# Kernel optimization log

Hardware: AMD Instinct MI355X
Metric: run time of the kernel (lower is better)

The kernel has to match this reference:

```python
import jax, jax.numpy as jnp
import numpy as np

B, N, D, H = 2, 2048, 1024, 16
HD = D // H

def setup_inputs() -> dict:
    key = jax.random.key(0)
    ks = jax.random.split(key, 8)
    s = lambda fan_in: 1.0 / np.sqrt(fan_in)
    return {
        "x": jax.random.normal(ks[0], (B, N, D), jnp.float32),
        "coverage": jax.random.uniform(ks[1], (B, N, 1), jnp.float32),
        "w_qkv": jax.random.normal(ks[2], (D, 3 * D), jnp.float32) * s(D),
        "w_out": jax.random.normal(ks[3], (D, D), jnp.float32) * s(D),
        "b_out": jnp.zeros((D,), jnp.float32),
        "w_ce1": jax.random.normal(ks[4], (1, D // 4), jnp.float32),
        "b_ce1": jnp.zeros((D // 4,), jnp.float32),
        "w_ce2": jax.random.normal(ks[5], (D // 4, H), jnp.float32) * s(D // 4),
        "b_ce2": jnp.zeros((H,), jnp.float32),
        "w_fg1": jax.random.normal(ks[6], (D, D // 4), jnp.float32) * s(D),
        "b_fg1": jnp.zeros((D // 4,), jnp.float32),
        "w_fg2": jax.random.normal(ks[7], (D // 4, 1), jnp.float32) * s(D // 4),
        "b_fg2": jnp.zeros((1,), jnp.float32),
    }

def reference(x, coverage, w_qkv, w_out, b_out, w_ce1, b_ce1, w_ce2, b_ce2,
              w_fg1, b_fg1, w_fg2, b_fg2):
    b, n, d = x.shape
    h = w_ce2.shape[1]
    hd = d // h
    scale = hd ** -0.5
    qkv = x @ w_qkv  # (B,N,3D)
    q, k, v = jnp.split(qkv, 3, axis=-1)
    q = q.reshape(b, n, h, hd).transpose(0, 2, 1, 3)  # (B,H,N,hd)
    k = k.reshape(b, n, h, hd).transpose(0, 2, 1, 3)
    v = v.reshape(b, n, h, hd).transpose(0, 2, 1, 3)
    attn = jnp.einsum("bhnd,bhmd->bhnm", q, k) * scale  # (B,H,N,N)
    # coverage bias: MLP(1 -> D/4 -> H), broadcast over query dim
    cov = jax.nn.silu(coverage @ w_ce1 + b_ce1) @ w_ce2 + b_ce2  # (B,N,H)
    cov_bias = cov.transpose(0, 2, 1)[:, :, None, :]  # (B,H,1,N)
    # fusion gate on mean-pooled features
    x_pooled = x.mean(axis=1)  # (B,D)
    g = jax.nn.sigmoid(jax.nn.silu(x_pooled @ w_fg1 + b_fg1) @ w_fg2 + b_fg2)  # (B,1)
    g = g[:, :, None, None]  # (B,1,1,1)
    # g*(attn+bias) + (1-g)*attn == attn + g*bias (exact same math)
    attn = attn + g * cov_bias
    attn = jax.nn.softmax(attn, axis=-1)
    out = jnp.einsum("bhnm,bhmd->bhnd", attn, v)  # (B,H,N,hd)
    out = out.transpose(0, 2, 1, 3).reshape(b, n, d)
    return out @ w_out + b_out
```

## Files before the change

### kernel.cpp

```cpp
#include <hip/hip_runtime.h>
#include <math.h>

typedef __bf16 bf16_t;
typedef __bf16 bf16x8 __attribute__((ext_vector_type(8)));
typedef __bf16 bf16x4 __attribute__((ext_vector_type(4)));
typedef float f32x4 __attribute__((ext_vector_type(4)));

#define MFMA16(a, b, c) __builtin_amdgcn_mfma_f32_16x16x32_bf16((a), (b), (c), 0, 0, 0)

constexpr int Bc = 2, Nc = 2048, Dc = 1024, Hc = 16, HDc = 64;
constexpr float C1 = 0.18033688011112042f;
constexpr float LOG2E = 1.4426950408889634f;

__device__ __forceinline__ void glds16(const bf16_t* g, bf16_t* l) {
    __builtin_amdgcn_global_load_lds(
        (const __attribute__((address_space(1))) unsigned int*)g,
        (__attribute__((address_space(3))) unsigned int*)l, 16, 0, 0);
}

__global__ __launch_bounds__(256) void prep_x(const float* __restrict__ x,
                                              bf16_t* __restrict__ Xb,
                                              float* __restrict__ pooled) {
    int row0 = blockIdx.x * 8;
    int b = row0 >> 11;
    int c = threadIdx.x * 4;
    float s0 = 0.f, s1 = 0.f, s2 = 0.f, s3 = 0.f;
#pragma unroll
    for (int rr = 0; rr < 8; ++rr) {
        size_t off = (size_t)(row0 + rr) * 1024 + c;
        float4 v = *(const float4*)(x + off);
        bf16x4 o = { (bf16_t)v.x, (bf16_t)v.y, (bf16_t)v.z, (bf16_t)v.w };
        *(bf16x4*)(Xb + off) = o;
        s0 += v.x; s1 += v.y; s2 += v.z; s3 += v.w;
    }
    atomicAdd(&pooled[b * 1024 + c + 0], s0);
    atomicAdd(&pooled[b * 1024 + c + 1], s1);
    atomicAdd(&pooled[b * 1024 + c + 2], s2);
    atomicAdd(&pooled[b * 1024 + c + 3], s3);
}

__global__ __launch_bounds__(256) void tr64f(const float* __restrict__ w_qkv,
                                             const float* __restrict__ w_out,
                                             bf16_t* __restrict__ Wt,
                                             bf16_t* __restrict__ WoT) {
    __shared__ bf16_t tile[64 * 66];
    const float* src; bf16_t* dst; int C, cx;
    if (blockIdx.x < 48) { src = w_qkv; dst = Wt; C = 3072; cx = blockIdx.x; }
    else                 { src = w_out; dst = WoT; C = 1024; cx = blockIdx.x - 48; }
    const int R = 1024;
    int r0 = blockIdx.y * 64, c0 = cx * 64;
    int t = threadIdx.x;
    int cl = t & 63, rl = t >> 6;
#pragma unroll
    for (int p = 0; p < 16; ++p) {
        int r = p * 4 + rl;
        tile[r * 66 + cl] = (bf16_t)src[(size_t)(r0 + r) * C + c0 + cl];
    }
    __syncthreads();
#pragma unroll
    for (int p = 0; p < 16; ++p) {
        int r = p * 4 + rl;
        dst[(size_t)(c0 + r) * R + r0 + cl] = tile[cl * 66 + r];
    }
}

__global__ __launch_bounds__(256) void gate1(const float* __restrict__ pooled,
                                             const float* __restrict__ w_fg1,
                                             const float* __restrict__ b_fg1,
                                             const float* __restrict__ w_fg2,
                                             float* __restrict__ hacc) {
    int b = blockIdx.x >> 8, j = blockIdx.x & 255;
    int t = threadIdx.x;
    float p = 0.f;
#pragma unroll
    for (int i = 0; i < 4; ++i) {
        int d = t * 4 + i;
        p += pooled[b * 1024 + d] * w_fg1[d * 256 + j];
    }
#pragma unroll
    for (int off = 32; off > 0; off >>= 1) p += __shfl_down(p, off);
    __shared__ float red[4];
    if ((t & 63) == 0) red[t >> 6] = p;
    __syncthreads();
    if (t == 0) {
        float hj = (red[0] + red[1] + red[2] + red[3]) * (1.0f / 2048.0f) + b_fg1[j];
        hj = hj / (1.0f + __expf(-hj));
        atomicAdd(&hacc[b], hj * w_fg2[j]);
    }
}

__global__ __launch_bounds__(256) void covbias_k(const float* __restrict__ coverage,
                                                 const float* __restrict__ w_ce1,
                                                 const float* __restrict__ b_ce1,
                                                 const float* __restrict__ w_ce2,
                                                 const float* __restrict__ b_ce2,
                                                 const float* __restrict__ hacc,
                                                 const float* __restrict__ b_fg2,
                                                 float* __restrict__ biasbuf) {
    int t = threadIdx.x;
    int h = t & 15;
    int gn = blockIdx.x * 16 + (t >> 4);
    int b = gn >> 11, n = gn & 2047;
    float g = 1.0f / (1.0f + __expf(-(hacc[b] + b_fg2[0])));
    float c = coverage[gn];
    float acc = b_ce2[h];
    for (int j = 0; j < 256; ++j) {
        float tv = c * w_ce1[j] + b_ce1[j];
        tv = tv / (1.0f + __expf(-tv));
        acc += tv * w_ce2[j * 16 + h];
    }
    biasbuf[((size_t)b * 16 + h) * 2048 + n] = LOG2E * g * acc;
}

__global__ __launch_bounds__(256) void qkv_gemm(const bf16_t* __restrict__ Xb,
                                                const bf16_t* __restrict__ Wt,
                                                bf16_t* __restrict__ Q,
                                                bf16_t* __restrict__ Kb,
                                                bf16_t* __restrict__ Vt) {
    __shared__ __align__(16) bf16_t At[128 * 32];
    __shared__ __align__(16) bf16_t Bt[128 * 32];
    int t = threadIdx.x, w = t >> 6, lane = t & 63;
    int l16 = lane & 15, quad = lane >> 4;
    int wm = w & 1, wx = w >> 1;
    int m0 = blockIdx.x * 128;
    int n0 = blockIdx.y * 128;
    f32x4 acc[4][4] = {};
    int sw = (l16 >> 2) & 3;

    for (int k0 = 0; k0 < 1024; k0 += 32) {
#pragma unroll
        for (int i = 0; i < 2; ++i) {
            int fb = i * 4096 + w * 1024;
            int f = fb + lane * 16;
            int row = f >> 6;
            int ch = (f >> 4) & 3;
            int sc = ch ^ ((row >> 2) & 3);
            glds16(Wt + (size_t)(n0 + row) * 1024 + k0 + sc * 8, At + (fb >> 1));
            glds16(Xb + (size_t)(m0 + row) * 1024 + k0 + sc * 8, Bt + (fb >> 1));
        }
        __syncthreads();
        bf16x8 afr[4], bfr[4];
#pragma unroll
        for (int mi = 0; mi < 4; ++mi)
            afr[mi] = *(const bf16x8*)(At + (wm * 64 + mi * 16 + l16) * 32 + ((quad ^ sw) * 8));
#pragma unroll
        for (int ni = 0; ni < 4; ++ni)
            bfr[ni] = *(const bf16x8*)(Bt + (wx * 64 + ni * 16 + l16) * 32 + ((quad ^ sw) * 8));
#pragma unroll
        for (int mi = 0; mi < 4; ++mi)
#pragma unroll
            for (int ni = 0; ni < 4; ++ni)
                acc[mi][ni] = MFMA16(afr[mi], bfr[ni], acc[mi][ni]);
        __syncthreads();
    }

    int sec = n0 >> 10;
#pragma unroll
    for (int mi = 0; mi < 4; ++mi) {
        int gc = n0 + wm * 64 + mi * 16 + quad * 4;
        int dcol = gc & 1023;
        int h = dcol >> 6, hd = dcol & 63;
#pragma unroll
        for (int ni = 0; ni < 4; ++ni) {
            int gx = m0 + wx * 64 + ni * 16 + l16;
            int b = gx >> 11, n = gx & 2047;
            size_t bh = (size_t)(b * 16 + h);
            if (sec == 2) {
                int np = (n & ~31) + ((n >> 2) & 3) * 8 + ((n >> 4) & 1) * 4 + (n & 3);
#pragma unroll
                for (int r = 0; r < 4; ++r)
                    Vt[(bh * 64 + hd + r) * 2048 + np] = (bf16_t)acc[mi][ni][r];
            } else {
                bf16x4 pk = { (bf16_t)acc[mi][ni][0], (bf16_t)acc[mi][ni][1],
                              (bf16_t)acc[mi][ni][2], (bf16_t)acc[mi][ni][3] };
                bf16_t* dst = (sec == 0 ? Q : Kb);
                *(bf16x4*)(dst + (bh * 2048 + n) * 64 + hd) = pk;
            }
        }
    }
}

__global__ __launch_bounds__(256) void attn_k(const bf16_t* __restrict__ Q,
                                              const bf16_t* __restrict__ Kb,
                                              const bf16_t* __restrict__ Vt,
                                              const float* __restrict__ biasbuf,
                                              bf16_t* __restrict__ O) {
    __shared__ __align__(16) bf16_t kbuf[2][64 * 64];
    __shared__ __align__(16) bf16_t vbuf[2][64 * 64];
    int t = threadIdx.x, w = t >> 6, lane = t & 63;
    int l16 = lane & 15, quad = lane >> 4;
    int bh = blockIdx.y;
    int b = bh >> 4, h = bh & 15;
    int qa = blockIdx.x * 128 + w * 32;
    const bf16_t* Qh = Q + (size_t)bh * 2048 * 64;
    const bf16_t* Kh = Kb + (size_t)bh * 2048 * 64;
    const bf16_t* Vh = Vt + (size_t)bh * 64 * 2048;
    const float* bih = biasbuf + (size_t)bh * 2048;

    int fb0 = w * 2048, fb1 = fb0 + 1024;
    int f0 = fb0 + lane * 16, f1 = fb1 + lane * 16;
    int krow0 = f0 >> 7, kch0 = ((f0 >> 4) & 7) ^ (krow0 & 7);
    int krow1 = f1 >> 7, kch1 = ((f1 >> 4) & 7) ^ (krow1 & 7);

    bf16x8 qf[2][2];
#pragma unroll
    for (int g = 0; g < 2; ++g)
#pragma unroll
        for (int dh = 0; dh < 2; ++dh)
            qf[g][dh] = *(const bf16x8*)(Qh + (size_t)(qa + g * 16 + l16) * 64 + dh * 32 + quad * 8);

    f32x4 o[2][4] = {};
    f32x4 osum[2] = {};
    const f32x4 zero = { 0.f, 0.f, 0.f, 0.f };
    int swl = l16 & 7;
    bf16x8 ones;
#pragma unroll
    for (int i = 0; i < 8; ++i) ones[i] = (bf16_t)1.0f;

    {
        glds16(Kh + (size_t)krow0 * 64 + kch0 * 8, &kbuf[0][fb0 >> 1]);
        glds16(Kh + (size_t)krow1 * 64 + kch1 * 8, &kbuf[0][fb1 >> 1]);
        glds16(Vh + (size_t)krow0 * 2048 + kch0 * 8, &vbuf[0][fb0 >> 1]);
        glds16(Vh + (size_t)krow1 * 2048 + kch1 * 8, &vbuf[0][fb1 >> 1]);
    }

    for (int it = 0; it < 32; ++it) {
        int j0 = it * 64, sel = it & 1;
        __syncthreads();
        if (it + 1 < 32) {
            int jn = j0 + 64, sn = sel ^ 1;
            glds16(Kh + (size_t)(jn + krow0) * 64 + kch0 * 8, &kbuf[sn][fb0 >> 1]);
            glds16(Kh + (size_t)(jn + krow1) * 64 + kch1 * 8, &kbuf[sn][fb1 >> 1]);
            glds16(Vh + (size_t)krow0 * 2048 + jn + kch0 * 8, &vbuf[sn][fb0 >> 1]);
            glds16(Vh + (size_t)krow1 * 2048 + jn + kch1 * 8, &vbuf[sn][fb1 >> 1]);
        }
        const bf16_t* kb = kbuf[sel];
        const bf16_t* vb = vbuf[sel];

        float4 bias[4];
#pragma unroll
        for (int kt = 0; kt < 4; ++kt)
            bias[kt] = *(const float4*)(bih + j0 + kt * 16 + quad * 4);

        f32x4 s[4][2];
#pragma unroll
        for (int kt = 0; kt < 4; ++kt) {
            bf16x8 kf0 = *(const bf16x8*)(kb + (kt * 16 + l16) * 64 + ((quad ^ swl) * 8));
            bf16x8 kf1 = *(const bf16x8*)(kb + (kt * 16 + l16) * 64 + (((4 + quad) ^ swl) * 8));
#pragma unroll
            for (int g = 0; g < 2; ++g) {
                s[kt][g] = MFMA16(kf0, qf[g][0], zero);
                s[kt][g] = MFMA16(kf1, qf[g][1], s[kt][g]);
            }
        }

#pragma unroll
        for (int kt = 0; kt < 4; ++kt) {
            const float* bp = (const float*)&bias[kt];
#pragma unroll
            for (int g = 0; g < 2; ++g)
#pragma unroll
                for (int r = 0; r < 4; ++r)
                    s[kt][g][r] = __builtin_amdgcn_exp2f(s[kt][g][r] * C1 + bp[r]);
        }

        bf16x8 pf[2][2];
#pragma unroll
        for (int g = 0; g < 2; ++g)
#pragma unroll
            for (int pv = 0; pv < 2; ++pv) {
                bf16x8 tmp;
#pragma unroll
                for (int i = 0; i < 4; ++i) {
                    tmp[i]     = (bf16_t)s[2 * pv][g][i];
                    tmp[i + 4] = (bf16_t)s[2 * pv + 1][g][i];
                }
                pf[g][pv] = tmp;
            }

#pragma unroll
        for (int dt = 0; dt < 4; ++dt) {
            const bf16_t* vrow = vb + (dt * 16 + l16) * 64;
#pragma unroll
            for (int pv = 0; pv < 2; ++pv) {
                bf16x8 vf = *(const bf16x8*)(vrow + (((pv * 4 + quad) ^ swl) * 8));
#pragma unroll
                for (int g = 0; g < 2; ++g)
                    o[g][dt] = MFMA16(pf[g][pv], vf, o[g][dt]);
            }
        }
#pragma unroll
        for (int g = 0; g < 2; ++g) {
            osum[g] = MFMA16(pf[g][0], ones, osum[g]);
            osum[g] = MFMA16(pf[g][1], ones, osum[g]);
        }
    }

#pragma unroll
    for (int g = 0; g < 2; ++g) {
        float rinv[4];
#pragma unroll
        for (int r = 0; r < 4; ++r) rinv[r] = 1.0f / osum[g][r];
#pragma unroll
        for (int dt = 0; dt < 4; ++dt)
#pragma unroll
            for (int r = 0; r < 4; ++r) {
                int row = qa + g * 16 + quad * 4 + r;
                O[(size_t)(b * 2048 + row) * 1024 + h * 64 + dt * 16 + l16] =
                    (bf16_t)(o[g][dt][r] * rinv[r]);
            }
    }
}

__global__ __launch_bounds__(256) void out_gemm(const bf16_t* __restrict__ A,
                                                const bf16_t* __restrict__ Wt,
                                                const float* __restrict__ bias,
                                                float* __restrict__ Cout) {
    __shared__ __align__(16) bf16_t At[64 * 32];
    __shared__ __align__(16) bf16_t Bt[128 * 32];
    int t = threadIdx.x, w = t >> 6, lane = t & 63;
    int l16 = lane & 15, quad = lane >> 4;
    int wm = w & 1, wx = w >> 1;
    int m0 = blockIdx.x * 128;
    int n0 = blockIdx.y * 64;
    f32x4 acc[2][4] = {};
    int sw = (l16 >> 2) & 3;

    for (int k0 = 0; k0 < 1024; k0 += 32) {
        {
            int fb = w * 1024;
            int f = fb + lane * 16;
            int row = f >> 6;
            int ch = (f >> 4) & 3;
            int sc = ch ^ ((row >> 2) & 3);
            glds16(Wt + (size_t)(n0 + row) * 1024 + k0 + sc * 8, At + (fb >> 1));
        }
#pragma unroll
        for (int i = 0; i < 2; ++i) {
            int fb = w * 2048 + i * 1024;
            int f = fb + lane * 16;
            int row = f >> 6;
            int ch = (f >> 4) & 3;
            int sc = ch ^ ((row >> 2) & 3);
            glds16(A + (size_t)(m0 + row) * 1024 + k0 + sc * 8, Bt + (fb >> 1));
        }
        __syncthreads();
        bf16x8 afr[2], bfr[4];
#pragma unroll
        for (int mi = 0; mi < 2; ++mi)
            afr[mi] = *(const bf16x8*)(At + (wm * 32 + mi * 16 + l16) * 32 + ((quad ^ sw) * 8));
#pragma unroll
        for (int ni = 0; ni < 4; ++ni)
            bfr[ni] = *(const bf16x8*)(Bt + (wx * 64 + ni * 16 + l16) * 32 + ((quad ^ sw) * 8));
#pragma unroll
        for (int mi = 0; mi < 2; ++mi)
#pragma unroll
            for (int ni = 0; ni < 4; ++ni)
                acc[mi][ni] = MFMA16(afr[mi], bfr[ni], acc[mi][ni]);
        __syncthreads();
    }

#pragma unroll
    for (int mi = 0; mi < 2; ++mi) {
        int gc = n0 + wm * 32 + mi * 16 + quad * 4;
        float4 bv = *(const float4*)(bias + gc);
#pragma unroll
        for (int ni = 0; ni < 4; ++ni) {
            int gx = m0 + wx * 64 + ni * 16 + l16;
            float4 ov = { acc[mi][ni][0] + bv.x, acc[mi][ni][1] + bv.y,
                          acc[mi][ni][2] + bv.z, acc[mi][ni][3] + bv.w };
            *(float4*)(Cout + (size_t)gx * 1024 + gc) = ov;
        }
    }
}

extern "C" void kernel_launch(void* const* d_in, const int* in_sizes, int n_in,
                              void* d_out, int out_size, void* d_ws, size_t ws_size,
                              hipStream_t stream) {
    const float* x     = (const float*)d_in[0];
    const float* cov   = (const float*)d_in[1];
    const float* w_qkv = (const float*)d_in[2];
    const float* w_out = (const float*)d_in[3];
    const float* b_out = (const float*)d_in[4];
    const float* w_ce1 = (const float*)d_in[5];
    const float* b_ce1 = (const float*)d_in[6];
    const float* w_ce2 = (const float*)d_in[7];
    const float* b_ce2 = (const float*)d_in[8];
    const float* w_fg1 = (const float*)d_in[9];
    const float* b_fg1 = (const float*)d_in[10];
    const float* w_fg2 = (const float*)d_in[11];
    const float* b_fg2 = (const float*)d_in[12];

    char* ws = (char*)d_ws;
    bf16_t* Wt     = (bf16_t*)(ws);
    bf16_t* WoT    = (bf16_t*)(ws + 6291456);
    bf16_t* Xb     = (bf16_t*)(ws + 8388608);
    bf16_t* Qb     = (bf16_t*)(ws + 16777216);
    bf16_t* Kbb    = (bf16_t*)(ws + 25165824);
    bf16_t* Vt     = (bf16_t*)(ws + 33554432);
    bf16_t* Ob     = (bf16_t*)(ws + 41943040);
    float*  pooled = (float*)(ws + 50331648);
    float*  hacc   = (float*)(ws + 50339840);
    float*  biasb  = (float*)(ws + 50340096);

    hipMemsetAsync(pooled, 0, 8192 + 256, stream);
    prep_x<<<512, 256, 0, stream>>>(x, Xb, pooled);
    tr64f<<<dim3(64, 16), 256, 0, stream>>>(w_qkv, w_out, Wt, WoT);
    gate1<<<512, 256, 0, stream>>>(pooled, w_fg1, b_fg1, w_fg2, hacc);
    covbias_k<<<256, 256, 0, stream>>>(cov, w_ce1, b_ce1, w_ce2, b_ce2, hacc, b_fg2, biasb);
    qkv_gemm<<<dim3(32, 24), 256, 0, stream>>>(Xb, Wt, Qb, Kbb, Vt);
    attn_k<<<dim3(16, 32), 256, 0, stream>>>(Qb, Kbb, Vt, biasb, Ob);
    out_gemm<<<dim3(32, 16), 256, 0, stream>>>(Ob, WoT, b_out, (float*)d_out);
}
```

Measured before the change: 272.1 us.

## Fuse prep kernels, move gate into attention, and double GEMM K-tile to 64

Merges x conversion/pooling, weight transposes and coverage-bias MLP into one launch, since the coverage bias no longer depends on the gate. The gate sigmoid is instead computed in the attention kernel and applied to the bias on load. Both GEMMs now stage 64-wide K tiles with an 8-way XOR swizzle, halving the number of barrier-separated iterations. This uses more LDS per block and adds a few multiplies per bias load in attention.

```diff
diff --git a/kernel.cpp b/kernel.cpp
--- a/kernel.cpp
+++ b/kernel.cpp
@@ -18,49 +18,71 @@
         (__attribute__((address_space(3))) unsigned int*)l, 16, 0, 0);
 }
 
-__global__ __launch_bounds__(256) void prep_x(const float* __restrict__ x,
-                                              bf16_t* __restrict__ Xb,
-                                              float* __restrict__ pooled) {
-    int row0 = blockIdx.x * 8;
-    int b = row0 >> 11;
-    int c = threadIdx.x * 4;
-    float s0 = 0.f, s1 = 0.f, s2 = 0.f, s3 = 0.f;
-#pragma unroll
-    for (int rr = 0; rr < 8; ++rr) {
-        size_t off = (size_t)(row0 + rr) * 1024 + c;
-        float4 v = *(const float4*)(x + off);
-        bf16x4 o = { (bf16_t)v.x, (bf16_t)v.y, (bf16_t)v.z, (bf16_t)v.w };
-        *(bf16x4*)(Xb + off) = o;
-        s0 += v.x; s1 += v.y; s2 += v.z; s3 += v.w;
-    }
-    atomicAdd(&pooled[b * 1024 + c + 0], s0);
-    atomicAdd(&pooled[b * 1024 + c + 1], s1);
-    atomicAdd(&pooled[b * 1024 + c + 2], s2);
-    atomicAdd(&pooled[b * 1024 + c + 3], s3);
-}
-
-__global__ __launch_bounds__(256) void tr64f(const float* __restrict__ w_qkv,
-                                             const float* __restrict__ w_out,
-                                             bf16_t* __restrict__ Wt,
-                                             bf16_t* __restrict__ WoT) {
+__global__ __launch_bounds__(256) void prep_all(const float* __restrict__ x,
+                                                const float* __restrict__ w_qkv,
+                                                const float* __restrict__ w_out,
+                                                const float* __restrict__ coverage,
+                                                const float* __restrict__ w_ce1,
+                                                const float* __restrict__ b_ce1,
+                                                const float* __restrict__ w_ce2,
+                                                const float* __restrict__ b_ce2,
+                                                bf16_t* __restrict__ Xb,
+                                                bf16_t* __restrict__ Wt,
+                                                bf16_t* __restrict__ WoT,
+                                                float* __restrict__ pooled,
+                                                float* __restrict__ biasbuf) {
     __shared__ bf16_t tile[64 * 66];
-    const float* src; bf16_t* dst; int C, cx;
-    if (blockIdx.x < 48) { src = w_qkv; dst = Wt; C = 3072; cx = blockIdx.x; }
-    else                 { src = w_out; dst = WoT; C = 1024; cx = blockIdx.x - 48; }
-    const int R = 1024;
-    int r0 = blockIdx.y * 64, c0 = cx * 64;
-    int t = threadIdx.x;
-    int cl = t & 63, rl = t >> 6;
-#pragma unroll
-    for (int p = 0; p < 16; ++p) {
-        int r = p * 4 + rl;
-        tile[r * 66 + cl] = (bf16_t)src[(size_t)(r0 + r) * C + c0 + cl];
-    }
-    __syncthreads();
-#pragma unroll
-    for (int p = 0; p < 16; ++p) {
-        int r = p * 4 + rl;
-        dst[(size_t)(c0 + r) * R + r0 + cl] = tile[cl * 66 + r];
+    int blk = blockIdx.x, t = threadIdx.x;
+    if (blk < 512) {
+        int row0 = blk * 8;
+        int b = row0 >> 11;
+        int c = t * 4;
+        float s0 = 0.f, s1 = 0.f, s2 = 0.f, s3 = 0.f;
+#pragma unroll
+        for (int rr = 0; rr < 8; ++rr) {
+            size_t off = (size_t)(row0 + rr) * 1024 + c;
+            float4 v = *(const float4*)(x + off);
+            bf16x4 o = { (bf16_t)v.x, (bf16_t)v.y, (bf16_t)v.z, (bf16_t)v.w };
+            *(bf16x4*)(Xb + off) = o;
+            s0 += v.x; s1 += v.y; s2 += v.z; s3 += v.w;
+        }
+        atomicAdd(&pooled[b * 1024 + c + 0], s0);
+        atomicAdd(&pooled[b * 1024 + c + 1], s1);
+        atomicAdd(&pooled[b * 1024 + c + 2], s2);
+        atomicAdd(&pooled[b * 1024 + c + 3], s3);
+    } else if (blk < 1536) {
+        int idx = blk - 512;
+        int cx = idx & 63, ry = idx >> 6;
+        const float* src; bf16_t* dst; int C;
+        if (cx < 48) { src = w_qkv; dst = Wt; C = 3072; }
+        else         { src = w_out; dst = WoT; C = 1024; cx -= 48; }
+        const int R = 1024;
+        int r0 = ry * 64, c0 = cx * 64;
+        int cl = t & 63, rl = t >> 6;
+#pragma unroll
+        for (int p = 0; p < 16; ++p) {
+            int r = p * 4 + rl;
+            tile[r * 66 + cl] = (bf16_t)src[(size_t)(r0 + r) * C + c0 + cl];
+        }
+        __syncthreads();
+#pragma unroll
+        for (int p = 0; p < 16; ++p) {
+            int r = p * 4 + rl;
+            dst[(size_t)(c0 + r) * R + r0 + cl] = tile[cl * 66 + r];
+        }
+    } else {
+        int cb = blk - 1536;
+        int h = t & 15;
+        int gn = cb * 16 + (t >> 4);
+        int b = gn >> 11, n = gn & 2047;
+        float c = coverage[gn];
+        float acc = b_ce2[h];
+        for (int j = 0; j < 256; ++j) {
+            float tv = c * w_ce1[j] + b_ce1[j];
+            tv = tv / (1.0f + __expf(-tv));
+            acc += tv * w_ce2[j * 16 + h];
+        }
+        biasbuf[((size_t)b * 16 + h) * 2048 + n] = LOG2E * acc;
     }
 }
 
@@ -89,68 +111,48 @@
     }
 }
 
-__global__ __launch_bounds__(256) void covbias_k(const float* __restrict__ coverage,
-                                                 const float* __restrict__ w_ce1,
-                                                 const float* __restrict__ b_ce1,
-                                                 const float* __restrict__ w_ce2,
-                                                 const float* __restrict__ b_ce2,
-                                                 const float* __restrict__ hacc,
-                                                 const float* __restrict__ b_fg2,
-                                                 float* __restrict__ biasbuf) {
-    int t = threadIdx.x;
-    int h = t & 15;
-    int gn = blockIdx.x * 16 + (t >> 4);
-    int b = gn >> 11, n = gn & 2047;
-    float g = 1.0f / (1.0f + __expf(-(hacc[b] + b_fg2[0])));
-    float c = coverage[gn];
-    float acc = b_ce2[h];
-    for (int j = 0; j < 256; ++j) {
-        float tv = c * w_ce1[j] + b_ce1[j];
-        tv = tv / (1.0f + __expf(-tv));
-        acc += tv * w_ce2[j * 16 + h];
-    }
-    biasbuf[((size_t)b * 16 + h) * 2048 + n] = LOG2E * g * acc;
-}
-
 __global__ __launch_bounds__(256) void qkv_gemm(const bf16_t* __restrict__ Xb,
                                                 const bf16_t* __restrict__ Wt,
                                                 bf16_t* __restrict__ Q,
                                                 bf16_t* __restrict__ Kb,
                                                 bf16_t* __restrict__ Vt) {
-    __shared__ __align__(16) bf16_t At[128 * 32];
-    __shared__ __align__(16) bf16_t Bt[128 * 32];
+    __shared__ __align__(16) bf16_t At[128 * 64];
+    __shared__ __align__(16) bf16_t Bt[128 * 64];
     int t = threadIdx.x, w = t >> 6, lane = t & 63;
     int l16 = lane & 15, quad = lane >> 4;
     int wm = w & 1, wx = w >> 1;
     int m0 = blockIdx.x * 128;
     int n0 = blockIdx.y * 128;
     f32x4 acc[4][4] = {};
-    int sw = (l16 >> 2) & 3;
-
-    for (int k0 = 0; k0 < 1024; k0 += 32) {
-#pragma unroll
-        for (int i = 0; i < 2; ++i) {
+    int swl = l16 & 7;
+
+    for (int k0 = 0; k0 < 1024; k0 += 64) {
+#pragma unroll
+        for (int i = 0; i < 4; ++i) {
             int fb = i * 4096 + w * 1024;
             int f = fb + lane * 16;
-            int row = f >> 6;
-            int ch = (f >> 4) & 3;
-            int sc = ch ^ ((row >> 2) & 3);
+            int row = f >> 7;
+            int ch = (f >> 4) & 7;
+            int sc = ch ^ (row & 7);
             glds16(Wt + (size_t)(n0 + row) * 1024 + k0 + sc * 8, At + (fb >> 1));
             glds16(Xb + (size_t)(m0 + row) * 1024 + k0 + sc * 8, Bt + (fb >> 1));
         }
         __syncthreads();
-        bf16x8 afr[4], bfr[4];
-#pragma unroll
-        for (int mi = 0; mi < 4; ++mi)
-            afr[mi] = *(const bf16x8*)(At + (wm * 64 + mi * 16 + l16) * 32 + ((quad ^ sw) * 8));
-#pragma unroll
-        for (int ni = 0; ni < 4; ++ni)
-            bfr[ni] = *(const bf16x8*)(Bt + (wx * 64 + ni * 16 + l16) * 32 + ((quad ^ sw) * 8));
-#pragma unroll
-        for (int mi = 0; mi < 4; ++mi)
+#pragma unroll
+        for (int s = 0; s < 2; ++s) {
+            bf16x8 afr[4], bfr[4];
+#pragma unroll
+            for (int mi = 0; mi < 4; ++mi)
+                afr[mi] = *(const bf16x8*)(At + (wm * 64 + mi * 16 + l16) * 64 + (((s * 4 + quad) ^ swl) * 8));
 #pragma unroll
             for (int ni = 0; ni < 4; ++ni)
-                acc[mi][ni] = MFMA16(afr[mi], bfr[ni], acc[mi][ni]);
+                bfr[ni] = *(const bf16x8*)(Bt + (wx * 64 + ni * 16 + l16) * 64 + (((s * 4 + quad) ^ swl) * 8));
+#pragma unroll
+            for (int mi = 0; mi < 4; ++mi)
+#pragma unroll
+                for (int ni = 0; ni < 4; ++ni)
+                    acc[mi][ni] = MFMA16(afr[mi], bfr[ni], acc[mi][ni]);
+        }
         __syncthreads();
     }
 
@@ -184,6 +186,8 @@
                                               const bf16_t* __restrict__ Kb,
                                               const bf16_t* __restrict__ Vt,
                                               const float* __restrict__ biasbuf,
+                                              const float* __restrict__ hacc,
+                                              const float* __restrict__ b_fg2,
                                               bf16_t* __restrict__ O) {
     __shared__ __align__(16) bf16_t kbuf[2][64 * 64];
     __shared__ __align__(16) bf16_t vbuf[2][64 * 64];
@@ -196,6 +200,7 @@
     const bf16_t* Kh = Kb + (size_t)bh * 2048 * 64;
     const bf16_t* Vh = Vt + (size_t)bh * 64 * 2048;
     const float* bih = biasbuf + (size_t)bh * 2048;
+    float gate = 1.0f / (1.0f + __expf(-(hacc[b] + b_fg2[0])));
 
     int fb0 = w * 2048, fb1 = fb0 + 1024;
     int f0 = fb0 + lane * 16, f1 = fb1 + lane * 16;
@@ -239,8 +244,11 @@
 
         float4 bias[4];
 #pragma unroll
-        for (int kt = 0; kt < 4; ++kt)
+        for (int kt = 0; kt < 4; ++kt) {
             bias[kt] = *(const float4*)(bih + j0 + kt * 16 + quad * 4);
+            bias[kt].x *= gate; bias[kt].y *= gate;
+            bias[kt].z *= gate; bias[kt].w *= gate;
+        }
 
         f32x4 s[4][2];
 #pragma unroll
@@ -316,47 +324,51 @@
                                                 const bf16_t* __restrict__ Wt,
                                                 const float* __restrict__ bias,
                                                 float* __restrict__ Cout) {
-    __shared__ __align__(16) bf16_t At[64 * 32];
-    __shared__ __align__(16) bf16_t Bt[128 * 32];
+    __shared__ __align__(16) bf16_t At[64 * 64];
+    __shared__ __align__(16) bf16_t Bt[128 * 64];
     int t = threadIdx.x, w = t >> 6, lane = t & 63;
     int l16 = lane & 15, quad = lane >> 4;
     int wm = w & 1, wx = w >> 1;
     int m0 = blockIdx.x * 128;
     int n0 = blockIdx.y * 64;
     f32x4 acc[2][4] = {};
-    int sw = (l16 >> 2) & 3;
-
-    for (int k0 = 0; k0 < 1024; k0 += 32) {
-        {
-            int fb = w * 1024;
+    int swl = l16 & 7;
+
+    for (int k0 = 0; k0 < 1024; k0 += 64) {
+#pragma unroll
+        for (int i = 0; i < 2; ++i) {
+            int fb = i * 4096 + w * 1024;
             int f = fb + lane * 16;
-            int row = f >> 6;
-            int ch = (f >> 4) & 3;
-            int sc = ch ^ ((row >> 2) & 3);
+            int row = f >> 7;
+            int ch = (f >> 4) & 7;
+            int sc = ch ^ (row & 7);
             glds16(Wt + (size_t)(n0 + row) * 1024 + k0 + sc * 8, At + (fb >> 1));
         }
 #pragma unroll
-        for (int i = 0; i < 2; ++i) {
-            int fb = w * 2048 + i * 1024;
+        for (int i = 0; i < 4; ++i) {
+            int fb = i * 4096 + w * 1024;
             int f = fb + lane * 16;
-            int row = f >> 6;
-            int ch = (f >> 4) & 3;
-            int sc = ch ^ ((row >> 2) & 3);
+            int row = f >> 7;
+            int ch = (f >> 4) & 7;
+            int sc = ch ^ (row & 7);
             glds16(A + (size_t)(m0 + row) * 1024 + k0 + sc * 8, Bt + (fb >> 1));
         }
         __syncthreads();
-        bf16x8 afr[2], bfr[4];
-#pragma unroll
-        for (int mi = 0; mi < 2; ++mi)
-            afr[mi] = *(const bf16x8*)(At + (wm * 32 + mi * 16 + l16) * 32 + ((quad ^ sw) * 8));
-#pragma unroll
-        for (int ni = 0; ni < 4; ++ni)
-            bfr[ni] = *(const bf16x8*)(Bt + (wx * 64 + ni * 16 + l16) * 32 + ((quad ^ sw) * 8));
-#pragma unroll
-        for (int mi = 0; mi < 2; ++mi)
+#pragma unroll
+        for (int s = 0; s < 2; ++s) {
+            bf16x8 afr[2], bfr[4];
+#pragma unroll
+            for (int mi = 0; mi < 2; ++mi)
+                afr[mi] = *(const bf16x8*)(At + (wm * 32 + mi * 16 + l16) * 64 + (((s * 4 + quad) ^ swl) * 8));
 #pragma unroll
             for (int ni = 0; ni < 4; ++ni)
-                acc[mi][ni] = MFMA16(afr[mi], bfr[ni], acc[mi][ni]);
+                bfr[ni] = *(const bf16x8*)(Bt + (wx * 64 + ni * 16 + l16) * 64 + (((s * 4 + quad) ^ swl) * 8));
+#pragma unroll
+            for (int mi = 0; mi < 2; ++mi)
+#pragma unroll
+                for (int ni = 0; ni < 4; ++ni)
+                    acc[mi][ni] = MFMA16(afr[mi], bfr[ni], acc[mi][ni]);
+        }
         __syncthreads();
     }
 
@@ -404,11 +416,10 @@
     float*  biasb  = (float*)(ws + 50340096);
 
     hipMemsetAsync(pooled, 0, 8192 + 256, stream);
-    prep_x<<<512, 256, 0, stream>>>(x, Xb, pooled);
-    tr64f<<<dim3(64, 16), 256, 0, stream>>>(w_qkv, w_out, Wt, WoT);
+    prep_all<<<1792, 256, 0, stream>>>(x, w_qkv, w_out, cov, w_ce1, b_ce1, w_ce2, b_ce2,
+                                       Xb, Wt, WoT, pooled, biasb);
     gate1<<<512, 256, 0, stream>>>(pooled, w_fg1, b_fg1, w_fg2, hacc);
-    covbias_k<<<256, 256, 0, stream>>>(cov, w_ce1, b_ce1, w_ce2, b_ce2, hacc, b_fg2, biasb);
     qkv_gemm<<<dim3(32, 24), 256, 0, stream>>>(Xb, Wt, Qb, Kbb, Vt);
-    attn_k<<<dim3(16, 32), 256, 0, stream>>>(Qb, Kbb, Vt, biasb, Ob);
+    attn_k<<<dim3(16, 32), 256, 0, stream>>>(Qb, Kbb, Vt, biasb, hacc, b_fg2, Ob);
     out_gemm<<<dim3(32, 16), 256, 0, stream>>>(Ob, WoT, b_out, (float*)d_out);
 }
```

Measured after the change: 281.8 us. +3.6%, slower.
